# Kernel optimization log

Measured on AMD Instinct MI355X. Metric: run time of the kernel, lower is better.

Reference implementation:

```python
import jax, jax.numpy as jnp
import numpy as np

# ODEBlock integrates dy/dt = f(t, y) from T0 to T1 with the dopri5 (Dormand-Prince RK45)
# stage structure. torchdiffeq's dopri5 is adaptive; for a jit/vjp-friendly reference we
# run the same 6-stage dopri5 tableau with a fixed number of steps (same per-step math).
T0, T1 = 0.0, 1.0
NUM_STEPS = 16

BATCH, D, H = 512, 1024, 2048


def setup_inputs() -> dict:
    key = jax.random.key(0)
    k0, k1, k2 = jax.random.split(key, 3)
    x = jax.random.normal(k0, (BATCH, D), dtype=jnp.float32)
    W1 = jax.random.normal(k1, (D, H), dtype=jnp.float32) / np.float32(np.sqrt(D))
    b1 = jnp.zeros((H,), dtype=jnp.float32)
    W2 = jax.random.normal(k2, (H, D), dtype=jnp.float32) / np.float32(np.sqrt(H))
    b2 = jnp.zeros((D,), dtype=jnp.float32)
    return {"x": x, "W1": W1, "b1": b1, "W2": W2, "b2": b2}


def reference(x, W1, b1, W2, b2):
    def f(t, y):
        # odefunc: 2-layer tanh MLP, autonomous in t
        return jnp.tanh(y @ W1 + b1) @ W2 + b2

    h = jnp.float32((T1 - T0) / NUM_STEPS)

    def step(carry, _):
        y, t = carry
        k1 = f(t, y)
        k2 = f(t + h * (1.0 / 5.0), y + h * (1.0 / 5.0) * k1)
        k3 = f(t + h * (3.0 / 10.0), y + h * ((3.0 / 40.0) * k1 + (9.0 / 40.0) * k2))
        k4 = f(t + h * (4.0 / 5.0),
               y + h * ((44.0 / 45.0) * k1 - (56.0 / 15.0) * k2 + (32.0 / 9.0) * k3))
        k5 = f(t + h * (8.0 / 9.0),
               y + h * ((19372.0 / 6561.0) * k1 - (25360.0 / 2187.0) * k2
                        + (64448.0 / 6561.0) * k3 - (212.0 / 729.0) * k4))
        k6 = f(t + h,
               y + h * ((9017.0 / 3168.0) * k1 - (355.0 / 33.0) * k2
                        + (46732.0 / 5247.0) * k3 + (49.0 / 176.0) * k4
                        - (5103.0 / 18656.0) * k5))
        # 5th-order solution weights (b7 = 0, so k7/FSAL not needed for the update)
        y_next = y + h * ((35.0 / 384.0) * k1 + (500.0 / 1113.0) * k3
                          + (125.0 / 192.0) * k4 - (2187.0 / 6784.0) * k5
                          + (11.0 / 84.0) * k6)
        return (y_next, t + h), None

    (y_final, _), _ = jax.lax.scan(step, (x, jnp.float32(T0)), None, length=NUM_STEPS)
    return y_final
```

## Files before the change

kernel.cpp:

```cpp
#include <hip/hip_runtime.h>
#include <hip/hip_bf16.h>

using bf16 = __hip_bfloat16;
typedef __attribute__((ext_vector_type(8))) short short8;
typedef __attribute__((ext_vector_type(4))) float f32x4;

#define MFMA16(A, B, C) __builtin_amdgcn_mfma_f32_16x16x32_bf16(A, B, C, 0, 0, 0)

constexpr int Mdim = 512;
constexpr int Ddim = 1024;
constexpr int Hdim = 2048;
constexpr size_t MH = (size_t)Mdim * Hdim;

constexpr double Hs = 1.0 / 16.0;
constexpr float CF[6][6] = {
    {float(Hs * 1 / 5.), 0.f, 0.f, 0.f, 0.f, 0.f},
    {float(Hs * 3 / 40.), float(Hs * 9 / 40.), 0.f, 0.f, 0.f, 0.f},
    {float(Hs * 44 / 45.), float(-Hs * 56 / 15.), float(Hs * 32 / 9.), 0.f, 0.f, 0.f},
    {float(Hs * 19372 / 6561.), float(-Hs * 25360 / 2187.), float(Hs * 64448 / 6561.),
     float(-Hs * 212 / 729.), 0.f, 0.f},
    {float(Hs * 9017 / 3168.), float(-Hs * 355 / 33.), float(Hs * 46732 / 5247.),
     float(Hs * 49 / 176.), float(-Hs * 5103 / 18656.), 0.f},
    {float(Hs * 35 / 384.), 0.f, float(Hs * 500 / 1113.), float(Hs * 125 / 192.),
     float(-Hs * 2187 / 6784.), float(Hs * 11 / 84.)},
};

__device__ __forceinline__ float tanh_fast(float x) {
  float xc = fminf(fmaxf(x, -15.0f), 15.0f);
  float t = __expf(2.0f * xc);
  return (t - 1.0f) * __builtin_amdgcn_rcpf(t + 1.0f);
}

__device__ __forceinline__ void gload_lds16(const void* g, void* lds) {
  __builtin_amdgcn_global_load_lds((const __attribute__((address_space(1))) void*)g,
                                   (__attribute__((address_space(3))) void*)lds, 16, 0, 0);
}

enum { M_PLAIN = 0, M_INIT = 1, M_STG = 2, M_FINAL = 3 };

struct GArgs {
  const bf16* A;
  const bf16* Bt;
  const float* b1;
  const float* b2w1;
  const float* xin;
  const float* b2;
  float* yW1;
  bf16* T;
  bf16* K;
  float* G;
  bf16* Wout;
  float* y;
};

template <int MODE, int STAGE, int NDIM, int KDIM>
__global__ __launch_bounds__(512, 2) void fused_gemm(GArgs a) {
  constexpr int BK = 128;
  constexpr int NITER = KDIM / BK;
  constexpr int NP = (NDIM / 64) / 8;

  extern __shared__ char smem_c[];

  const int tid = threadIdx.x;
  const int lane = tid & 63;
  const int wid = tid >> 6;
  const int kq = wid & 3;
  const int nh = wid >> 2;
  const int fr = lane & 15;
  const int kg = (lane >> 4) & 3;

  const int bid = blockIdx.x;
  const int nt = (bid & 7) * NP + ((bid >> 3) % NP);
  const int mt = (bid >> 3) / NP;
  const int brow = mt * 64, bcol = nt * 64;

  const int rs0 = tid >> 4;
  const int cgS = (tid & 15) ^ (rs0 & 7);
  const bf16* pA0 = a.A + (size_t)(brow + rs0) * KDIM + cgS * 8;
  const bf16* pA1 = pA0 + (size_t)32 * KDIM;
  const bf16* pB0 = a.Bt + (size_t)(bcol + rs0) * KDIM + cgS * 8;
  const bf16* pB1 = pB0 + (size_t)32 * KDIM;
  char* dA = smem_c + tid * 16;
  char* dB = smem_c + 16384 + tid * 16;

#define STAGE_TILE(T_)                                                       \
  {                                                                          \
    const int B_ = ((T_) % 3) * 32768;                                       \
    const int KO_ = (T_)*BK;                                                 \
    gload_lds16(pA0 + KO_, dA + B_); gload_lds16(pA1 + KO_, dA + B_ + 8192); \
    gload_lds16(pB0 + KO_, dB + B_); gload_lds16(pB1 + KO_, dB + B_ + 8192); \
  }

  const int xA = (((kq * 4 + kg) ^ (fr & 7)) << 4);
  const char* rA = smem_c + fr * 256 + xA;
  const char* rB = smem_c + 16384 + (nh * 32 + fr) * 256 + xA;

  f32x4 acc[4][2] = {};

  STAGE_TILE(0)
  STAGE_TILE(1)

#pragma unroll
  for (int t = 0; t < NITER; ++t) {
    if (t < NITER - 1) asm volatile("s_waitcnt vmcnt(4)" ::: "memory");
    else               asm volatile("s_waitcnt vmcnt(0)" ::: "memory");
    __builtin_amdgcn_s_barrier();
    __builtin_amdgcn_sched_barrier(0);
    if (t + 2 < NITER) STAGE_TILE(t + 2)
    const int BO = (t % 3) * 32768;
    short8 af[4], bw[2];
    af[0] = *(const short8*)(rA + BO);
    af[1] = *(const short8*)(rA + BO + 4096);
    af[2] = *(const short8*)(rA + BO + 8192);
    af[3] = *(const short8*)(rA + BO + 12288);
    bw[0] = *(const short8*)(rB + BO);
    bw[1] = *(const short8*)(rB + BO + 4096);
    __builtin_amdgcn_s_setprio(1);
#pragma unroll
    for (int mf = 0; mf < 4; ++mf)
#pragma unroll
      for (int nf = 0; nf < 2; ++nf) acc[mf][nf] = MFMA16(af[mf], bw[nf], acc[mf][nf]);
    __builtin_amdgcn_s_setprio(0);
  }
#undef STAGE_TILE

  __syncthreads();
#pragma unroll
  for (int mf = 0; mf < 4; ++mf)
#pragma unroll
    for (int nf = 0; nf < 2; ++nf)
      *(f32x4*)(smem_c + (((mf * 4 + nh * 2 + nf) * 4 + kq) << 10) + lane * 16) = acc[mf][nf];
  __syncthreads();

#pragma unroll
  for (int of = 0; of < 2; ++of) {
    const int p = wid * 2 + of;
    const int mfo = p >> 2, nfo = p & 3;
    f32x4 s = {};
#pragma unroll
    for (int k = 0; k < 4; ++k)
      s += *(const f32x4*)(smem_c + (((p * 4 + k) << 10)) + lane * 16);

    const int c = bcol + nfo * 16 + fr;
    const int r0 = brow + mfo * 16 + kg * 4;
#pragma unroll
    for (int e = 0; e < 4; ++e) {
      const int r = r0 + e;
      const size_t idx = (size_t)r * NDIM + c;
      const float cvv = s[e];
      if constexpr (MODE == M_PLAIN) {
        a.Wout[idx] = __float2bfloat16(cvv);
      } else if constexpr (MODE == M_INIT) {
        a.yW1[idx] = cvv;
        const float tv = tanh_fast(cvv + a.b1[c]);
        a.T[idx] = __float2bfloat16(tv);
        a.G[idx] = CF[5][0] * tv;
      } else if constexpr (MODE == M_STG) {
        const float Kv = cvv + a.b2w1[c];
        if constexpr (STAGE <= 5) a.K[(size_t)(STAGE - 1) * MH + idx] = __float2bfloat16(Kv);
        float comb = a.yW1[idx] + CF[STAGE - 1][STAGE - 1] * Kv;
        if constexpr (STAGE > 1 && CF[STAGE - 1][0] != 0.f)
          comb += CF[STAGE - 1][0] * __bfloat162float(a.K[0 * MH + idx]);
        if constexpr (STAGE > 2 && CF[STAGE - 1][1] != 0.f)
          comb += CF[STAGE - 1][1] * __bfloat162float(a.K[1 * MH + idx]);
        if constexpr (STAGE > 3 && CF[STAGE - 1][2] != 0.f)
          comb += CF[STAGE - 1][2] * __bfloat162float(a.K[2 * MH + idx]);
        if constexpr (STAGE > 4 && CF[STAGE - 1][3] != 0.f)
          comb += CF[STAGE - 1][3] * __bfloat162float(a.K[3 * MH + idx]);
        if constexpr (STAGE > 5 && CF[STAGE - 1][4] != 0.f)
          comb += CF[STAGE - 1][4] * __bfloat162float(a.K[4 * MH + idx]);
        if constexpr (STAGE < 6) {
          const float tv = tanh_fast(comb + a.b1[c]);
          a.T[idx] = __float2bfloat16(tv);
          if constexpr (CF[5][STAGE] != 0.f) a.G[idx] += CF[5][STAGE] * tv;
        } else {
          a.yW1[idx] = comb;
          const float tv = tanh_fast(comb + a.b1[c]);
          a.T[idx] = __float2bfloat16(tv);
          a.G[idx] += CF[5][0] * tv;
        }
      } else {
        a.y[idx] = a.xin[idx] + cvv + a.b2[c];
      }
    }
  }
}

__global__ void transpose_to_bf16(const float* __restrict__ in, bf16* __restrict__ out, int R,
                                  int C) {
  __shared__ float t[32][33];
  const int c0 = blockIdx.x * 32, r0 = blockIdx.y * 32;
#pragma unroll
  for (int i = threadIdx.y; i < 32; i += 8)
    t[i][threadIdx.x] = in[(size_t)(r0 + i) * C + c0 + threadIdx.x];
  __syncthreads();
#pragma unroll
  for (int i = threadIdx.y; i < 32; i += 8)
    out[(size_t)(c0 + i) * R + r0 + threadIdx.x] = __float2bfloat16(t[threadIdx.x][i]);
}

__global__ void cast_bf16(const float* __restrict__ in, bf16* __restrict__ out, int n4) {
  int i = blockIdx.x * 256 + threadIdx.x;
  if (i < n4) {
    float4 v = *(const float4*)(in + i * 4);
    bf16* o = out + i * 4;
    o[0] = __float2bfloat16(v.x); o[1] = __float2bfloat16(v.y);
    o[2] = __float2bfloat16(v.z); o[3] = __float2bfloat16(v.w);
  }
}

__global__ void b2w1_kernel(const float* __restrict__ b2, const float* __restrict__ W1,
                            float* __restrict__ out) {
  const int h = blockIdx.x * 256 + threadIdx.x;
  float s = 0.f;
  for (int d = 0; d < Ddim; ++d) s += b2[d] * W1[(size_t)d * Hdim + h];
  out[h] = s;
}

extern "C" void kernel_launch(void* const* d_in, const int* in_sizes, int n_in, void* d_out,
                              int out_size, void* d_ws, size_t ws_size, hipStream_t stream) {
  const float* x = (const float*)d_in[0];
  const float* W1 = (const float*)d_in[1];
  const float* b1 = (const float*)d_in[2];
  const float* W2 = (const float*)d_in[3];
  const float* b2 = (const float*)d_in[4];
  float* y = (float*)d_out;

  char* ws = (char*)d_ws;
  bf16* W1t = (bf16*)(ws + 0);
  bf16* W2bf = (bf16*)(ws + (4ull << 20));
  bf16* W2t = (bf16*)(ws + (8ull << 20));
  bf16* W21t = (bf16*)(ws + (12ull << 20));
  bf16* xbf = (bf16*)(ws + (20ull << 20));
  bf16* Tbuf = (bf16*)(ws + (21ull << 20));
  bf16* Kbuf = (bf16*)(ws + (23ull << 20));
  bf16* Gbf = (bf16*)(ws + (33ull << 20));
  float* yW1 = (float*)(ws + (35ull << 20));
  float* Gacc = (float*)(ws + (39ull << 20));
  float* b2w1 = (float*)(ws + (43ull << 20));

  GArgs a = {};
  a.b1 = b1; a.b2w1 = b2w1; a.xin = x; a.b2 = b2;
  a.yW1 = yW1; a.T = Tbuf; a.K = Kbuf; a.G = Gacc; a.y = y;

  constexpr int SMEM = 98304;
  hipFuncSetAttribute((const void*)&fused_gemm<M_PLAIN, 0, Hdim, 1024>,
                      hipFuncAttributeMaxDynamicSharedMemorySize, SMEM);
  hipFuncSetAttribute((const void*)&fused_gemm<M_INIT, 0, Hdim, 1024>,
                      hipFuncAttributeMaxDynamicSharedMemorySize, SMEM);
  hipFuncSetAttribute((const void*)&fused_gemm<M_STG, 1, Hdim, Hdim>,
                      hipFuncAttributeMaxDynamicSharedMemorySize, SMEM);
  hipFuncSetAttribute((const void*)&fused_gemm<M_STG, 2, Hdim, Hdim>,
                      hipFuncAttributeMaxDynamicSharedMemorySize, SMEM);
  hipFuncSetAttribute((const void*)&fused_gemm<M_STG, 3, Hdim, Hdim>,
                      hipFuncAttributeMaxDynamicSharedMemorySize, SMEM);
  hipFuncSetAttribute((const void*)&fused_gemm<M_STG, 4, Hdim, Hdim>,
                      hipFuncAttributeMaxDynamicSharedMemorySize, SMEM);
  hipFuncSetAttribute((const void*)&fused_gemm<M_STG, 5, Hdim, Hdim>,
                      hipFuncAttributeMaxDynamicSharedMemorySize, SMEM);
  hipFuncSetAttribute((const void*)&fused_gemm<M_STG, 6, Hdim, Hdim>,
                      hipFuncAttributeMaxDynamicSharedMemorySize, SMEM);
  hipFuncSetAttribute((const void*)&fused_gemm<M_FINAL, 0, Ddim, Hdim>,
                      hipFuncAttributeMaxDynamicSharedMemorySize, SMEM);

  transpose_to_bf16<<<dim3(Hdim / 32, Ddim / 32), dim3(32, 8), 0, stream>>>(W1, W1t, Ddim, Hdim);
  transpose_to_bf16<<<dim3(Ddim / 32, Hdim / 32), dim3(32, 8), 0, stream>>>(W2, W2t, Hdim, Ddim);
  cast_bf16<<<(Hdim * Ddim / 4 + 255) / 256, 256, 0, stream>>>(W2, W2bf, Hdim * Ddim / 4);
  cast_bf16<<<(Mdim * Ddim / 4 + 255) / 256, 256, 0, stream>>>(x, xbf, Mdim * Ddim / 4);
  b2w1_kernel<<<Hdim / 256, 256, 0, stream>>>(b2, W1, b2w1);

  {
    GArgs p = a; p.A = W1t; p.Bt = W2bf; p.Wout = W21t;
    fused_gemm<M_PLAIN, 0, Hdim, 1024><<<32 * 32, 512, SMEM, stream>>>(p);
  }
  {
    GArgs p = a; p.A = xbf; p.Bt = W1t;
    fused_gemm<M_INIT, 0, Hdim, 1024><<<8 * 32, 512, SMEM, stream>>>(p);
  }

  GArgs sg = a; sg.A = Tbuf; sg.Bt = W21t;
  for (int step = 0; step < 16; ++step) {
    fused_gemm<M_STG, 1, Hdim, Hdim><<<8 * 32, 512, SMEM, stream>>>(sg);
    fused_gemm<M_STG, 2, Hdim, Hdim><<<8 * 32, 512, SMEM, stream>>>(sg);
    fused_gemm<M_STG, 3, Hdim, Hdim><<<8 * 32, 512, SMEM, stream>>>(sg);
    fused_gemm<M_STG, 4, Hdim, Hdim><<<8 * 32, 512, SMEM, stream>>>(sg);
    fused_gemm<M_STG, 5, Hdim, Hdim><<<8 * 32, 512, SMEM, stream>>>(sg);
    if (step < 15)
      fused_gemm<M_STG, 6, Hdim, Hdim><<<8 * 32, 512, SMEM, stream>>>(sg);
  }

  cast_bf16<<<(int)(MH / 4 + 255) / 256, 256, 0, stream>>>(Gacc, Gbf, (int)(MH / 4));
  {
    GArgs p = a; p.A = Gbf; p.Bt = W2t;
    fused_gemm<M_FINAL, 0, Ddim, Hdim><<<8 * 16, 512, SMEM, stream>>>(p);
  }
}
```

Baseline: 1.423 ms.

## Split-K stage GEMMs into two halves with ticket-based partial-sum reduction

Replaces the per-stage GEMM kernel with a dedicated kernel that tiles 64x128 output blocks and splits the K dimension (2048) into two halves, each handled by a separate workgroup. Each half writes its partial sum to a workspace buffer, and an atomic ticket decides which of the two workgroups adds the other's partial and runs the fused RK epilogue. It also uses a three-deep LDS buffer with 147KB shared memory. The goal is shorter per-workgroup K loops and a deeper load pipeline, paid for with extra global traffic for partials, atomics, and reduced occupancy from the larger LDS footprint.

```diff
diff --git a/kernel.cpp b/kernel.cpp
--- a/kernel.cpp
+++ b/kernel.cpp
@@ -51,7 +51,169 @@
   float* G;
   bf16* Wout;
   float* y;
+  float* part;
+  int* tkt;
 };
+
+template <int STAGE>
+__device__ __forceinline__ void stage_epilogue(const GArgs& a, float cvv, int r, int c) {
+  const size_t idx = (size_t)r * Hdim + c;
+  const float Kv = cvv + a.b2w1[c];
+  if constexpr (STAGE <= 5) a.K[(size_t)(STAGE - 1) * MH + idx] = __float2bfloat16(Kv);
+  float comb = a.yW1[idx] + CF[STAGE - 1][STAGE - 1] * Kv;
+  if constexpr (STAGE > 1 && CF[STAGE - 1][0] != 0.f)
+    comb += CF[STAGE - 1][0] * __bfloat162float(a.K[0 * MH + idx]);
+  if constexpr (STAGE > 2 && CF[STAGE - 1][1] != 0.f)
+    comb += CF[STAGE - 1][1] * __bfloat162float(a.K[1 * MH + idx]);
+  if constexpr (STAGE > 3 && CF[STAGE - 1][2] != 0.f)
+    comb += CF[STAGE - 1][2] * __bfloat162float(a.K[2 * MH + idx]);
+  if constexpr (STAGE > 4 && CF[STAGE - 1][3] != 0.f)
+    comb += CF[STAGE - 1][3] * __bfloat162float(a.K[3 * MH + idx]);
+  if constexpr (STAGE > 5 && CF[STAGE - 1][4] != 0.f)
+    comb += CF[STAGE - 1][4] * __bfloat162float(a.K[4 * MH + idx]);
+  if constexpr (STAGE < 6) {
+    const float tv = tanh_fast(comb + a.b1[c]);
+    a.T[idx] = __float2bfloat16(tv);
+    if constexpr (CF[5][STAGE] != 0.f) a.G[idx] += CF[5][STAGE] * tv;
+  } else {
+    a.yW1[idx] = comb;
+    const float tv = tanh_fast(comb + a.b1[c]);
+    a.T[idx] = __float2bfloat16(tv);
+    a.G[idx] += CF[5][0] * tv;
+  }
+}
+
+template <int STAGE>
+__global__ __launch_bounds__(512, 2) void fused_stage(GArgs a) {
+  constexpr int NITER = 8;
+  extern __shared__ char smem_c[];
+
+  const int tid = threadIdx.x;
+  const int lane = tid & 63;
+  const int wid = tid >> 6;
+  const int kq = wid & 3;
+  const int nh = wid >> 2;
+  const int fr = lane & 15;
+  const int kg = (lane >> 4) & 3;
+
+  const int bid = blockIdx.x;
+  const int idx = bid >> 3;
+  const int nt = (bid & 7) * 2 + (idx & 1);
+  const int kh = (idx >> 1) & 1;
+  const int mt = idx >> 2;
+  const int brow = mt * 64, bcol = nt * 128;
+
+  const int rs0 = tid >> 4;
+  const int cg = (tid & 15) ^ (rs0 & 7);
+  const bf16* pA0 = a.A + ((size_t)(brow + rs0) << 11) + kh * 1024 + cg * 8;
+  const bf16* pA1 = pA0 + ((size_t)32 << 11);
+  const bf16* pB0 = a.Bt + ((size_t)(bcol + rs0) << 11) + kh * 1024 + cg * 8;
+  const bf16* pB1 = pB0 + ((size_t)32 << 11);
+  const bf16* pB2 = pB0 + ((size_t)64 << 11);
+  const bf16* pB3 = pB0 + ((size_t)96 << 11);
+  char* dA = smem_c + tid * 16;
+  char* dB = smem_c + 16384 + tid * 16;
+
+#define STG(T_)                                                                   \
+  {                                                                               \
+    constexpr int B_ = ((T_) % 3) * 49152;                                        \
+    constexpr int KO_ = (T_)*128;                                                 \
+    gload_lds16(pA0 + KO_, dA + B_);         gload_lds16(pA1 + KO_, dA + B_ + 8192); \
+    gload_lds16(pB0 + KO_, dB + B_);         gload_lds16(pB1 + KO_, dB + B_ + 8192); \
+    gload_lds16(pB2 + KO_, dB + B_ + 16384); gload_lds16(pB3 + KO_, dB + B_ + 24576); \
+  }
+
+  const int xc = (((kq * 4 + kg) ^ (fr & 7)) << 4);
+  const char* rA = smem_c + fr * 256 + xc;
+  const char* rB = smem_c + 16384 + (nh * 64 + fr) * 256 + xc;
+
+  f32x4 acc[4][4] = {};
+  STG(0) STG(1)
+
+#pragma unroll
+  for (int t = 0; t < NITER; ++t) {
+    if (t < NITER - 1) asm volatile("s_waitcnt vmcnt(6)" ::: "memory");
+    else               asm volatile("s_waitcnt vmcnt(0)" ::: "memory");
+    __builtin_amdgcn_s_barrier();
+    __builtin_amdgcn_sched_barrier(0);
+    switch (t + 2) {
+      case 2: STG(2) break; case 3: STG(3) break; case 4: STG(4) break;
+      case 5: STG(5) break; case 6: STG(6) break; case 7: STG(7) break;
+      default: break;
+    }
+    const int BO = (t % 3) * 49152;
+    short8 af[4], bw[4];
+    af[0] = *(const short8*)(rA + BO);
+    af[1] = *(const short8*)(rA + BO + 4096);
+    af[2] = *(const short8*)(rA + BO + 8192);
+    af[3] = *(const short8*)(rA + BO + 12288);
+    bw[0] = *(const short8*)(rB + BO);
+    bw[1] = *(const short8*)(rB + BO + 4096);
+    bw[2] = *(const short8*)(rB + BO + 8192);
+    bw[3] = *(const short8*)(rB + BO + 12288);
+    __builtin_amdgcn_s_setprio(1);
+#pragma unroll
+    for (int mf = 0; mf < 4; ++mf)
+#pragma unroll
+      for (int nf = 0; nf < 4; ++nf) acc[mf][nf] = MFMA16(af[mf], bw[nf], acc[mf][nf]);
+    __builtin_amdgcn_s_setprio(0);
+  }
+#undef STG
+
+  __syncthreads();
+#pragma unroll
+  for (int mf = 0; mf < 4; ++mf)
+#pragma unroll
+    for (int nf = 0; nf < 4; ++nf)
+      *(f32x4*)(smem_c + (((mf * 8 + nh * 4 + nf) * 4 + kq) << 10) + lane * 16) = acc[mf][nf];
+  __syncthreads();
+
+  f32x4 sum[4];
+#pragma unroll
+  for (int of = 0; of < 4; ++of) {
+    const int p = wid * 4 + of;
+    f32x4 s = {};
+#pragma unroll
+    for (int k = 0; k < 4; ++k)
+      s += *(const f32x4*)(smem_c + (((p * 4 + k) << 10)) + lane * 16);
+    sum[of] = s;
+  }
+
+  const int tile = mt * 16 + nt;
+  float* own = a.part + ((size_t)(tile * 2 + kh)) * 8192;
+  float* other = a.part + ((size_t)(tile * 2 + (1 - kh))) * 8192;
+  int* flg = a.tkt + tile;
+#pragma unroll
+  for (int of = 0; of < 4; ++of)
+    *(f32x4*)(own + (wid * 4 + of) * 256 + lane * 4) = sum[of];
+  __syncthreads();
+  int* sh = (int*)(smem_c + 131072);
+  if (tid == 0) {
+    __threadfence();
+    int old = atomicAdd(flg, 1);
+    if (old == 1) {
+      __threadfence();
+      atomicExch(flg, 0);
+    }
+    *sh = old;
+  }
+  __syncthreads();
+  if (*sh == 0) return;
+
+#pragma unroll
+  for (int of = 0; of < 4; ++of)
+    sum[of] += *(const f32x4*)(other + (wid * 4 + of) * 256 + lane * 4);
+
+#pragma unroll
+  for (int of = 0; of < 4; ++of) {
+    const int p = wid * 4 + of;
+    const int mfo = p >> 3, nfr = p & 7;
+    const int c = bcol + nfr * 16 + fr;
+    const int r0 = brow + mfo * 16 + kg * 4;
+#pragma unroll
+    for (int e = 0; e < 4; ++e) stage_epilogue<STAGE>(a, sum[of][e], r0 + e, c);
+  }
+}
 
 template <int MODE, int STAGE, int NDIM, int KDIM>
 __global__ __launch_bounds__(512, 2) void fused_gemm(GArgs a) {
@@ -155,30 +317,6 @@
         const float tv = tanh_fast(cvv + a.b1[c]);
         a.T[idx] = __float2bfloat16(tv);
         a.G[idx] = CF[5][0] * tv;
-      } else if constexpr (MODE == M_STG) {
-        const float Kv = cvv + a.b2w1[c];
-        if constexpr (STAGE <= 5) a.K[(size_t)(STAGE - 1) * MH + idx] = __float2bfloat16(Kv);
-        float comb = a.yW1[idx] + CF[STAGE - 1][STAGE - 1] * Kv;
-        if constexpr (STAGE > 1 && CF[STAGE - 1][0] != 0.f)
-          comb += CF[STAGE - 1][0] * __bfloat162float(a.K[0 * MH + idx]);
-        if constexpr (STAGE > 2 && CF[STAGE - 1][1] != 0.f)
-          comb += CF[STAGE - 1][1] * __bfloat162float(a.K[1 * MH + idx]);
-        if constexpr (STAGE > 3 && CF[STAGE - 1][2] != 0.f)
-          comb += CF[STAGE - 1][2] * __bfloat162float(a.K[2 * MH + idx]);
-        if constexpr (STAGE > 4 && CF[STAGE - 1][3] != 0.f)
-          comb += CF[STAGE - 1][3] * __bfloat162float(a.K[3 * MH + idx]);
-        if constexpr (STAGE > 5 && CF[STAGE - 1][4] != 0.f)
-          comb += CF[STAGE - 1][4] * __bfloat162float(a.K[4 * MH + idx]);
-        if constexpr (STAGE < 6) {
-          const float tv = tanh_fast(comb + a.b1[c]);
-          a.T[idx] = __float2bfloat16(tv);
-          if constexpr (CF[5][STAGE] != 0.f) a.G[idx] += CF[5][STAGE] * tv;
-        } else {
-          a.yW1[idx] = comb;
-          const float tv = tanh_fast(comb + a.b1[c]);
-          a.T[idx] = __float2bfloat16(tv);
-          a.G[idx] += CF[5][0] * tv;
-        }
       } else {
         a.y[idx] = a.xin[idx] + cvv + a.b2[c];
       }
@@ -238,31 +376,36 @@
   float* yW1 = (float*)(ws + (35ull << 20));
   float* Gacc = (float*)(ws + (39ull << 20));
   float* b2w1 = (float*)(ws + (43ull << 20));
+  int* tkt = (int*)(ws + (43ull << 20) + 16384);
+  float* part = (float*)(ws + (44ull << 20));
 
   GArgs a = {};
   a.b1 = b1; a.b2w1 = b2w1; a.xin = x; a.b2 = b2;
   a.yW1 = yW1; a.T = Tbuf; a.K = Kbuf; a.G = Gacc; a.y = y;
+  a.part = part; a.tkt = tkt;
 
   constexpr int SMEM = 98304;
+  constexpr int SMEM_STG = 147456;
   hipFuncSetAttribute((const void*)&fused_gemm<M_PLAIN, 0, Hdim, 1024>,
                       hipFuncAttributeMaxDynamicSharedMemorySize, SMEM);
   hipFuncSetAttribute((const void*)&fused_gemm<M_INIT, 0, Hdim, 1024>,
                       hipFuncAttributeMaxDynamicSharedMemorySize, SMEM);
-  hipFuncSetAttribute((const void*)&fused_gemm<M_STG, 1, Hdim, Hdim>,
-                      hipFuncAttributeMaxDynamicSharedMemorySize, SMEM);
-  hipFuncSetAttribute((const void*)&fused_gemm<M_STG, 2, Hdim, Hdim>,
-                      hipFuncAttributeMaxDynamicSharedMemorySize, SMEM);
-  hipFuncSetAttribute((const void*)&fused_gemm<M_STG, 3, Hdim, Hdim>,
-                      hipFuncAttributeMaxDynamicSharedMemorySize, SMEM);
-  hipFuncSetAttribute((const void*)&fused_gemm<M_STG, 4, Hdim, Hdim>,
-                      hipFuncAttributeMaxDynamicSharedMemorySize, SMEM);
-  hipFuncSetAttribute((const void*)&fused_gemm<M_STG, 5, Hdim, Hdim>,
-                      hipFuncAttributeMaxDynamicSharedMemorySize, SMEM);
-  hipFuncSetAttribute((const void*)&fused_gemm<M_STG, 6, Hdim, Hdim>,
-                      hipFuncAttributeMaxDynamicSharedMemorySize, SMEM);
   hipFuncSetAttribute((const void*)&fused_gemm<M_FINAL, 0, Ddim, Hdim>,
                       hipFuncAttributeMaxDynamicSharedMemorySize, SMEM);
-
+  hipFuncSetAttribute((const void*)&fused_stage<1>, hipFuncAttributeMaxDynamicSharedMemorySize,
+                      SMEM_STG);
+  hipFuncSetAttribute((const void*)&fused_stage<2>, hipFuncAttributeMaxDynamicSharedMemorySize,
+                      SMEM_STG);
+  hipFuncSetAttribute((const void*)&fused_stage<3>, hipFuncAttributeMaxDynamicSharedMemorySize,
+                      SMEM_STG);
+  hipFuncSetAttribute((const void*)&fused_stage<4>, hipFuncAttributeMaxDynamicSharedMemorySize,
+                      SMEM_STG);
+  hipFuncSetAttribute((const void*)&fused_stage<5>, hipFuncAttributeMaxDynamicSharedMemorySize,
+                      SMEM_STG);
+  hipFuncSetAttribute((const void*)&fused_stage<6>, hipFuncAttributeMaxDynamicSharedMemorySize,
+                      SMEM_STG);
+
+  hipMemsetAsync(tkt, 0, 1024, stream);
   transpose_to_bf16<<<dim3(Hdim / 32, Ddim / 32), dim3(32, 8), 0, stream>>>(W1, W1t, Ddim, Hdim);
   transpose_to_bf16<<<dim3(Ddim / 32, Hdim / 32), dim3(32, 8), 0, stream>>>(W2, W2t, Hdim, Ddim);
   cast_bf16<<<(Hdim * Ddim / 4 + 255) / 256, 256, 0, stream>>>(W2, W2bf, Hdim * Ddim / 4);
@@ -280,13 +423,13 @@
 
   GArgs sg = a; sg.A = Tbuf; sg.Bt = W21t;
   for (int step = 0; step < 16; ++step) {
-    fused_gemm<M_STG, 1, Hdim, Hdim><<<8 * 32, 512, SMEM, stream>>>(sg);
-    fused_gemm<M_STG, 2, Hdim, Hdim><<<8 * 32, 512, SMEM, stream>>>(sg);
-    fused_gemm<M_STG, 3, Hdim, Hdim><<<8 * 32, 512, SMEM, stream>>>(sg);
-    fused_gemm<M_STG, 4, Hdim, Hdim><<<8 * 32, 512, SMEM, stream>>>(sg);
-    fused_gemm<M_STG, 5, Hdim, Hdim><<<8 * 32, 512, SMEM, stream>>>(sg);
+    fused_stage<1><<<256, 512, SMEM_STG, stream>>>(sg);
+    fused_stage<2><<<256, 512, SMEM_STG, stream>>>(sg);
+    fused_stage<3><<<256, 512, SMEM_STG, stream>>>(sg);
+    fused_stage<4><<<256, 512, SMEM_STG, stream>>>(sg);
+    fused_stage<5><<<256, 512, SMEM_STG, stream>>>(sg);
     if (step < 15)
-      fused_gemm<M_STG, 6, Hdim, Hdim><<<8 * 32, 512, SMEM, stream>>>(sg);
+      fused_stage<6><<<256, 512, SMEM_STG, stream>>>(sg);
   }
 
   cast_bf16<<<(int)(MH / 4 + 255) / 256, 256, 0, stream>>>(Gacc, Gbf, (int)(MH / 4));
```

After: 3.012 ms. 112% more time.
